# Performance work log

Hardware: AMD Instinct MI355X
Metric: run time of the kernel (lower is better)

## Reference

```python
import jax, jax.numpy as jnp
import numpy as np

N, D, H, O, P = 50000, 256, 512, 64, 1024


def setup_inputs() -> dict:
    key = jax.random.key(0)
    ks = jax.random.split(key, 9)
    x = jax.random.normal(ks[0], (N, D), dtype=jnp.float32)
    W1 = jax.random.normal(ks[1], (H, D), dtype=jnp.float32) / np.sqrt(D)
    b1 = jax.random.normal(ks[2], (H,), dtype=jnp.float32) * 0.01
    W2 = jax.random.normal(ks[3], (O, H), dtype=jnp.float32) / np.sqrt(H)
    b2 = jax.random.normal(ks[4], (O,), dtype=jnp.float32) * 0.01
    ap = jax.random.randint(ks[5], (P,), 0, N, dtype=jnp.int32)
    p = jax.random.randint(ks[6], (P,), 0, N, dtype=jnp.int32)
    an = jax.random.randint(ks[7], (P,), 0, N, dtype=jnp.int32)
    n = jax.random.randint(ks[8], (P,), 0, N, dtype=jnp.int32)
    return {"x": x, "W1": W1, "b1": b1, "W2": W2, "b2": b2,
            "ap": ap, "p": p, "an": an, "n": n}


def reference(x, W1, b1, W2, b2, ap, p, an, n):
    """ContrastiveHessianCalculator.compute_hessian, loss_func='contrastive_full',
    wrt='weight', shape='diagonal', speed='half' (exact GGN diag), for the nnj net
    Linear(D,H) -> Tanh -> Linear(H,O).

    For a pair (x1,x2) the combined diag m0 - 2*m1 + m2 equals
    diag((J1-J2)^T (J1-J2)) where Ji = d f(xi)/d params. Closed form per layer:
      W1[i,j]: S11_i*x1_j^2 - 2*S12_i*x1_j*x2_j + S22_i*x2_j^2,
               Sab_i = tanh'(z1a)_i * tanh'(z1b)_i * sum_o W2[o,i]^2
      b1[i]:   S11_i - 2*S12_i + S22_i
      W2[i,j]: (h1_j - h2_j)^2  (independent of output row i)
      b2[i]:   0  (bias Jacobians of the two branches cancel)
    Per-layer diags are flattened [weight, bias] and concatenated (torch.cat(.., dim=1)),
    then summed over the pair batch; return sum(pos) - sum(neg).
    """
    c = jnp.sum(W2 * W2, axis=0)  # [H]

    def pair_hess_diag(ia, ib):
        xa = x[ia]            # [P, D]
        xb = x[ib]            # [P, D]
        ha = jnp.tanh(xa @ W1.T + b1)   # [P, H]
        hb = jnp.tanh(xb @ W1.T + b1)
        da = 1.0 - ha * ha              # tanh' at x_a, [P, H]
        db = 1.0 - hb * hb
        S11 = da * da * c               # [P, H]
        S12 = da * db * c
        S22 = db * db * c
        # W1 diag: [P, H, D]
        W1d = (S11[:, :, None] * (xa * xa)[:, None, :]
               - 2.0 * S12[:, :, None] * (xa * xb)[:, None, :]
               + S22[:, :, None] * (xb * xb)[:, None, :])
        b1d = S11 - 2.0 * S12 + S22      # [P, H]
        hd = (ha - hb) ** 2              # [P, H]
        W2d = jnp.broadcast_to(hd[:, None, :], (hd.shape[0], O, H))  # [P, O, H]
        b2d = jnp.zeros((hd.shape[0], O), dtype=hd.dtype)
        flat = jnp.concatenate([W1d.reshape(hd.shape[0], -1), b1d,
                                W2d.reshape(hd.shape[0], -1), b2d], axis=1)
        return jnp.sum(flat, axis=0)     # sum over pair batch -> [n_params]

    pos = pair_hess_diag(ap, p)
    neg = pair_hess_diag(an, n)
    return pos - neg
```

## Files before the change

kernel.cpp:

```cpp
#include <hip/hip_runtime.h>
#include <math.h>

#define DD_ 256
#define HH_ 512
#define OO_ 64

typedef __attribute__((ext_vector_type(8))) short bf16x8s;
typedef __attribute__((ext_vector_type(4))) float f32x4;

__device__ __forceinline__ unsigned short f2bf(float f) {
    unsigned u = __float_as_uint(f);
    u += 0x7FFF + ((u >> 16) & 1);
    return (unsigned short)(u >> 16);
}
__device__ __forceinline__ float bf2f(unsigned short h) {
    return __uint_as_float(((unsigned)h) << 16);
}
__device__ __forceinline__ int swz4(int r, int g) {
    return g ^ (r & 3) ^ ((r >> 2) & 3);
}
__device__ __forceinline__ float fast_tanh(float z) {
    float e = __expf(2.f * z);
    return 1.f - __fdividef(2.f, e + 1.f);
}

__global__ __launch_bounds__(256) void k_mega(
    const float* __restrict__ x, const float* __restrict__ W1,
    const float* __restrict__ b1, const float* __restrict__ W2,
    const int* __restrict__ ap, const int* __restrict__ pI,
    const int* __restrict__ an, const int* __restrict__ nI,
    short* __restrict__ Mt, short* __restrict__ Xt,
    float* __restrict__ pb1, float* __restrict__ phd) {
    const int t = threadIdx.x;
    const int bb = blockIdx.x;
    if (bb < 512) {
        __shared__ short Ah[64 * 32], Al[64 * 32], Bh[64 * 32], Bl[64 * 32];
        __shared__ float ht[64][67];
        __shared__ int sidx[64];
        const int n0 = (bb & 7) * 64;
        const int ry = bb >> 3;
        const int s = ry >> 5;
        const int p0 = (ry & 31) * 32;
        const int* IA = s ? an : ap;
        const int* IB = s ? nI : pI;
        if (t < 32) sidx[t] = IA[p0 + t];
        else if (t < 64) sidx[t] = IB[p0 + t - 32];
        __syncthreads();
        const int row = t >> 2, q = t & 3;
        const int l = t & 63, w = t >> 6;
        const int wm = w >> 1, wn = w & 1;
        const int lm = l & 15, g = l >> 4;
        const int sw = swz4(row, q);
        const float* srcA = x + (size_t)sidx[row] * DD_ + q * 8;
        const float* srcB = W1 + (size_t)(n0 + row) * DD_ + q * 8;
        float4 pa0 = *(const float4*)srcA;
        float4 pa1 = *(const float4*)(srcA + 4);
        float4 pb0 = *(const float4*)srcB;
        float4 pb1v = *(const float4*)(srcB + 4);
        f32x4 acc[2][2] = {};
        for (int k0 = 0; k0 < DD_; k0 += 32) {
            {
                float f[8] = {pa0.x, pa0.y, pa0.z, pa0.w, pa1.x, pa1.y, pa1.z, pa1.w};
                bf16x8s hi, lo;
                #pragma unroll
                for (int e = 0; e < 8; ++e) {
                    unsigned short hh = f2bf(f[e]);
                    hi[e] = (short)hh;
                    lo[e] = (short)f2bf(f[e] - bf2f(hh));
                }
                *(bf16x8s*)(&Ah[(row * 4 + sw) * 8]) = hi;
                *(bf16x8s*)(&Al[(row * 4 + sw) * 8]) = lo;
            }
            {
                float f[8] = {pb0.x, pb0.y, pb0.z, pb0.w, pb1v.x, pb1v.y, pb1v.z, pb1v.w};
                bf16x8s hi, lo;
                #pragma unroll
                for (int e = 0; e < 8; ++e) {
                    unsigned short hh = f2bf(f[e]);
                    hi[e] = (short)hh;
                    lo[e] = (short)f2bf(f[e] - bf2f(hh));
                }
                *(bf16x8s*)(&Bh[(row * 4 + sw) * 8]) = hi;
                *(bf16x8s*)(&Bl[(row * 4 + sw) * 8]) = lo;
            }
            __syncthreads();
            if (k0 + 32 < DD_) {
                pa0 = *(const float4*)(srcA + k0 + 32);
                pa1 = *(const float4*)(srcA + k0 + 36);
                pb0 = *(const float4*)(srcB + k0 + 32);
                pb1v = *(const float4*)(srcB + k0 + 36);
            }
            bf16x8s ah[2], al[2], bh[2], bl[2];
            #pragma unroll
            for (int mi = 0; mi < 2; ++mi) {
                int r = wm * 32 + mi * 16 + lm;
                ah[mi] = *(const bf16x8s*)(&Ah[(r * 4 + swz4(r, g)) * 8]);
                al[mi] = *(const bf16x8s*)(&Al[(r * 4 + swz4(r, g)) * 8]);
            }
            #pragma unroll
            for (int nj = 0; nj < 2; ++nj) {
                int r = wn * 32 + nj * 16 + lm;
                bh[nj] = *(const bf16x8s*)(&Bh[(r * 4 + swz4(r, g)) * 8]);
                bl[nj] = *(const bf16x8s*)(&Bl[(r * 4 + swz4(r, g)) * 8]);
            }
            #pragma unroll
            for (int mi = 0; mi < 2; ++mi)
                #pragma unroll
                for (int nj = 0; nj < 2; ++nj) {
                    acc[mi][nj] = __builtin_amdgcn_mfma_f32_16x16x32_bf16(ah[mi], bh[nj], acc[mi][nj], 0, 0, 0);
                    acc[mi][nj] = __builtin_amdgcn_mfma_f32_16x16x32_bf16(ah[mi], bl[nj], acc[mi][nj], 0, 0, 0);
                    acc[mi][nj] = __builtin_amdgcn_mfma_f32_16x16x32_bf16(al[mi], bh[nj], acc[mi][nj], 0, 0, 0);
                }
            __syncthreads();
        }
        #pragma unroll
        for (int mi = 0; mi < 2; ++mi)
            #pragma unroll
            for (int nj = 0; nj < 2; ++nj) {
                int jl = wn * 32 + nj * 16 + lm;
                float bv = b1[n0 + jl];
                #pragma unroll
                for (int qq = 0; qq < 4; ++qq) {
                    int r = wm * 32 + mi * 16 + g * 4 + qq;
                    ht[r][jl] = fast_tanh(acc[mi][nj][qq] + bv);
                }
            }
        __syncthreads();
        const int il = t >> 2, pq = t & 3;
        float ci = 0.f;
        #pragma unroll 8
        for (int o = 0; o < OO_; ++o) { float wv = W2[o * HH_ + n0 + il]; ci += wv * wv; }
        const float sgn = s ? -1.f : 1.f;
        float b1p = 0.f, hdp = 0.f;
        bf16x8s v0, v1, v2;
        #pragma unroll
        for (int pp = 0; pp < 8; ++pp) {
            int pl = pq * 8 + pp;
            float ha = ht[pl][il];
            float hb = ht[pl + 32][il];
            float da = 1.f - ha * ha, db = 1.f - hb * hb;
            float s11 = sgn * (da * da * ci);
            float s12 = sgn * (-2.f * da * db * ci);
            float s22 = sgn * (db * db * ci);
            v0[pp] = (short)f2bf(s11);
            v1[pp] = (short)f2bf(s12);
            v2[pp] = (short)f2bf(s22);
            b1p += s11 + s12 + s22;
            float d = ha - hb;
            hdp += sgn * d * d;
        }
        size_t base = (size_t)(n0 + il) * 6144 + s * 1024 + p0 + pq * 8;
        *(bf16x8s*)(&Mt[base]) = v0;
        *(bf16x8s*)(&Mt[base + 2048]) = v1;
        *(bf16x8s*)(&Mt[base + 4096]) = v2;
        b1p += __shfl_xor(b1p, 1); b1p += __shfl_xor(b1p, 2);
        hdp += __shfl_xor(hdp, 1); hdp += __shfl_xor(hdp, 2);
        if (pq == 0) { pb1[ry * HH_ + n0 + il] = b1p; phd[ry * HH_ + n0 + il] = hdp; }
    } else {
        __shared__ int sia[64], sib[64];
        const int b2 = bb - 512;
        const int jblk = b2 >> 5, pblk = b2 & 31;
        const int j = jblk * 64 + (t >> 2), pq = t & 3;
        const int p0 = pblk * 64;
        const int s = p0 >> 10;
        const int* IA = s ? an : ap;
        const int* IB = s ? nI : pI;
        if (t < 64) sia[t] = IA[(p0 & 1023) + t];
        else if (t < 128) sib[t - 64] = IB[(p0 & 1023) + (t - 64)];
        __syncthreads();
        short xv[3][16];
        #pragma unroll
        for (int pp = 0; pp < 16; ++pp) {
            int pl = pq * 16 + pp;
            float xa = x[(size_t)sia[pl] * DD_ + j];
            float xb = x[(size_t)sib[pl] * DD_ + j];
            xv[0][pp] = (short)f2bf(xa * xa);
            xv[1][pp] = (short)f2bf(xa * xb);
            xv[2][pp] = (short)f2bf(xb * xb);
        }
        size_t base = (size_t)j * 6144 + p0 + pq * 16;
        #pragma unroll
        for (int term = 0; term < 3; ++term) {
            bf16x8s v0, v1;
            #pragma unroll
            for (int e = 0; e < 8; ++e) { v0[e] = xv[term][e]; v1[e] = xv[term][e + 8]; }
            *(bf16x8s*)(&Xt[base + (size_t)term * 2048]) = v0;
            *(bf16x8s*)(&Xt[base + (size_t)term * 2048 + 8]) = v1;
        }
    }
}

__global__ __launch_bounds__(256) void k_gemm2(
    const short* __restrict__ Mt, const short* __restrict__ Xt,
    float* __restrict__ part) {
    __shared__ short As[64 * 32], Bs[64 * 32];
    const int t = threadIdx.x;
    const int j0 = blockIdx.x * 64;
    const int i0 = blockIdx.y * 64;
    const int kb = blockIdx.z;
    const int row = t >> 2, q = t & 3;
    const int l = t & 63, w = t >> 6;
    const int wm = w >> 1, wn = w & 1;
    const int lm = l & 15, g = l >> 4;
    const int sw = swz4(row, q);
    const short* srcA = &Mt[(size_t)(i0 + row) * 6144 + kb * 384 + q * 8];
    const short* srcB = &Xt[(size_t)(j0 + row) * 6144 + kb * 384 + q * 8];
    bf16x8s ra = *(const bf16x8s*)srcA;
    bf16x8s rb = *(const bf16x8s*)srcB;
    f32x4 acc[2][2] = {};
    for (int ks = 0; ks < 12; ++ks) {
        *(bf16x8s*)(&As[(row * 4 + sw) * 8]) = ra;
        *(bf16x8s*)(&Bs[(row * 4 + sw) * 8]) = rb;
        __syncthreads();
        if (ks < 11) {
            ra = *(const bf16x8s*)(srcA + (ks + 1) * 32);
            rb = *(const bf16x8s*)(srcB + (ks + 1) * 32);
        }
        bf16x8s a[2], b[2];
        #pragma unroll
        for (int mi = 0; mi < 2; ++mi) {
            int r = wm * 32 + mi * 16 + lm;
            a[mi] = *(const bf16x8s*)(&As[(r * 4 + swz4(r, g)) * 8]);
        }
        #pragma unroll
        for (int nj = 0; nj < 2; ++nj) {
            int r = wn * 32 + nj * 16 + lm;
            b[nj] = *(const bf16x8s*)(&Bs[(r * 4 + swz4(r, g)) * 8]);
        }
        #pragma unroll
        for (int mi = 0; mi < 2; ++mi)
            #pragma unroll
            for (int nj = 0; nj < 2; ++nj)
                acc[mi][nj] = __builtin_amdgcn_mfma_f32_16x16x32_bf16(a[mi], b[nj], acc[mi][nj], 0, 0, 0);
        __syncthreads();
    }
    #pragma unroll
    for (int mi = 0; mi < 2; ++mi)
        #pragma unroll
        for (int nj = 0; nj < 2; ++nj) {
            int j = j0 + wn * 32 + nj * 16 + lm;
            #pragma unroll
            for (int qq = 0; qq < 4; ++qq) {
                int i = i0 + wm * 32 + mi * 16 + g * 4 + qq;
                part[((size_t)kb * HH_ + i) * DD_ + j] = acc[mi][nj][qq];
            }
        }
}

__global__ void k_tail(const float* __restrict__ part, const float* __restrict__ pb1,
                       const float* __restrict__ phd, float* __restrict__ out) {
    const int gid = blockIdx.x * 256 + threadIdx.x;
    const int HD4 = 32768;
    f32x4* out4 = (f32x4*)out;
    if (gid < HD4) {
        f32x4 sv = {};
        #pragma unroll
        for (int kb = 0; kb < 16; ++kb)
            sv += *(const f32x4*)(&part[(size_t)kb * 131072 + gid * 4]);
        out4[gid] = sv;
    } else if (gid < HD4 + 128) {
        const int i4 = gid - HD4;
        f32x4 sv = {};
        for (int k2 = 0; k2 < 64; ++k2)
            sv += *(const f32x4*)(&pb1[k2 * HH_ + i4 * 4]);
        out4[HD4 + i4] = sv;
    } else if (gid < HD4 + 256) {
        const int i4 = gid - HD4 - 128;
        f32x4 sv = {};
        for (int k2 = 0; k2 < 64; ++k2)
            sv += *(const f32x4*)(&phd[k2 * HH_ + i4 * 4]);
        #pragma unroll 8
        for (int o = 0; o < OO_; ++o)
            out4[HD4 + 128 + o * 128 + i4] = sv;
    } else if (gid < HD4 + 272) {
        f32x4 z = {};
        out4[41088 + gid - HD4 - 256] = z;
    }
}

extern "C" void kernel_launch(void* const* d_in, const int* in_sizes, int n_in,
                              void* d_out, int out_size, void* d_ws, size_t ws_size,
                              hipStream_t stream) {
    const float* x  = (const float*)d_in[0];
    const float* W1 = (const float*)d_in[1];
    const float* b1 = (const float*)d_in[2];
    const float* W2 = (const float*)d_in[3];
    const int* ap = (const int*)d_in[5];
    const int* pI = (const int*)d_in[6];
    const int* an = (const int*)d_in[7];
    const int* nI = (const int*)d_in[8];
    float* out = (float*)d_out;
    float* ws = (float*)d_ws;

    float* part = ws;
    short* Mt   = (short*)(ws + 2097152);
    short* Xt   = (short*)(ws + 3670016);
    float* pb1  = ws + 4456448;
    float* phd  = ws + 4489216;

    k_mega<<<dim3(640), dim3(256), 0, stream>>>(x, W1, b1, W2, ap, pI, an, nI,
                                                Mt, Xt, pb1, phd);
    k_gemm2<<<dim3(4, 8, 16), dim3(256), 0, stream>>>(Mt, Xt, part);
    k_tail<<<dim3(130), dim3(256), 0, stream>>>(part, pb1, phd, out);
}
```

Before: 33.81 us.

## Double-buffer LDS tiles, pack bf16 conversions, fold Xt production into GEMM1 blocks

Both GEMM loops now use double-buffered shared memory, so each iteration needs one barrier instead of two and the next tile's conversion and store overlap the current MFMAs. The fp32-to-bf16 hi/lo split uses packed two-element conversion intrinsics. The separate 128 blocks that built the Xt squared-input matrix are removed, and every one of the 512 GEMM1 blocks now also writes a quarter of an Xt tile, which balances work across blocks. The cost is twice the shared memory per block and smaller 8-byte Xt stores with indices read straight from global memory.

```diff
diff --git a/kernel.cpp b/kernel.cpp
--- a/kernel.cpp
+++ b/kernel.cpp
@@ -1,4 +1,5 @@
 #include <hip/hip_runtime.h>
+#include <hip/hip_bf16.h>
 #include <math.h>
 
 #define DD_ 256
@@ -6,15 +7,31 @@
 #define OO_ 64
 
 typedef __attribute__((ext_vector_type(8))) short bf16x8s;
+typedef __attribute__((ext_vector_type(4))) short bf16x4s;
 typedef __attribute__((ext_vector_type(4))) float f32x4;
+typedef __attribute__((ext_vector_type(4))) unsigned int u32x4;
 
 __device__ __forceinline__ unsigned short f2bf(float f) {
     unsigned u = __float_as_uint(f);
     u += 0x7FFF + ((u >> 16) & 1);
     return (unsigned short)(u >> 16);
 }
-__device__ __forceinline__ float bf2f(unsigned short h) {
-    return __uint_as_float(((unsigned)h) << 16);
+__device__ __forceinline__ unsigned pk2(float a, float b) {
+    __hip_bfloat162 h = __float22bfloat162_rn(make_float2(a, b));
+    return *reinterpret_cast<unsigned*>(&h);
+}
+__device__ __forceinline__ void cvt8hl(const float4& v0, const float4& v1,
+                                       u32x4& hi, u32x4& lo) {
+    float f[8] = {v0.x, v0.y, v0.z, v0.w, v1.x, v1.y, v1.z, v1.w};
+    #pragma unroll
+    for (int e = 0; e < 4; ++e) {
+        float a = f[2 * e], b = f[2 * e + 1];
+        unsigned h = pk2(a, b);
+        float ra = a - __uint_as_float(h << 16);
+        float rb = b - __uint_as_float(h & 0xFFFF0000u);
+        hi[e] = h;
+        lo[e] = pk2(ra, rb);
+    }
 }
 __device__ __forceinline__ int swz4(int r, int g) {
     return g ^ (r & 3) ^ ((r >> 2) & 3);
@@ -31,101 +48,95 @@
     const int* __restrict__ an, const int* __restrict__ nI,
     short* __restrict__ Mt, short* __restrict__ Xt,
     float* __restrict__ pb1, float* __restrict__ phd) {
+    __shared__ short Ah[2][64 * 32], Al[2][64 * 32];
+    __shared__ short Bh[2][64 * 32], Bl[2][64 * 32];
+    __shared__ float ht[64][67];
+    __shared__ int sidx[64];
     const int t = threadIdx.x;
     const int bb = blockIdx.x;
-    if (bb < 512) {
-        __shared__ short Ah[64 * 32], Al[64 * 32], Bh[64 * 32], Bl[64 * 32];
-        __shared__ float ht[64][67];
-        __shared__ int sidx[64];
-        const int n0 = (bb & 7) * 64;
-        const int ry = bb >> 3;
-        const int s = ry >> 5;
-        const int p0 = (ry & 31) * 32;
-        const int* IA = s ? an : ap;
-        const int* IB = s ? nI : pI;
-        if (t < 32) sidx[t] = IA[p0 + t];
-        else if (t < 64) sidx[t] = IB[p0 + t - 32];
+    const int n0 = (bb & 7) * 64;
+    const int ry = bb >> 3;
+    const int s = ry >> 5;
+    const int p0 = (ry & 31) * 32;
+    const int* IA = s ? an : ap;
+    const int* IB = s ? nI : pI;
+    if (t < 32) sidx[t] = IA[p0 + t];
+    else if (t < 64) sidx[t] = IB[p0 + t - 32];
+    __syncthreads();
+    const int row = t >> 2, q = t & 3;
+    const int l = t & 63, w = t >> 6;
+    const int wm = w >> 1, wn = w & 1;
+    const int lm = l & 15, g = l >> 4;
+    const int sw = swz4(row, q);
+    const int stIdx = (row * 4 + sw) * 8;
+    const float* srcA = x + (size_t)sidx[row] * DD_ + q * 8;
+    const float* srcB = W1 + (size_t)(n0 + row) * DD_ + q * 8;
+    {
+        float4 a0 = *(const float4*)srcA;
+        float4 a1 = *(const float4*)(srcA + 4);
+        float4 b0 = *(const float4*)srcB;
+        float4 b1q = *(const float4*)(srcB + 4);
+        u32x4 hi, lo;
+        cvt8hl(a0, a1, hi, lo);
+        *(u32x4*)(&Ah[0][stIdx]) = hi; *(u32x4*)(&Al[0][stIdx]) = lo;
+        cvt8hl(b0, b1q, hi, lo);
+        *(u32x4*)(&Bh[0][stIdx]) = hi; *(u32x4*)(&Bl[0][stIdx]) = lo;
+    }
+    f32x4 acc[2][2] = {};
+    #pragma unroll 2
+    for (int ks = 0; ks < 8; ++ks) {
+        const int cur = ks & 1;
         __syncthreads();
-        const int row = t >> 2, q = t & 3;
-        const int l = t & 63, w = t >> 6;
-        const int wm = w >> 1, wn = w & 1;
-        const int lm = l & 15, g = l >> 4;
-        const int sw = swz4(row, q);
-        const float* srcA = x + (size_t)sidx[row] * DD_ + q * 8;
-        const float* srcB = W1 + (size_t)(n0 + row) * DD_ + q * 8;
-        float4 pa0 = *(const float4*)srcA;
-        float4 pa1 = *(const float4*)(srcA + 4);
-        float4 pb0 = *(const float4*)srcB;
-        float4 pb1v = *(const float4*)(srcB + 4);
-        f32x4 acc[2][2] = {};
-        for (int k0 = 0; k0 < DD_; k0 += 32) {
-            {
-                float f[8] = {pa0.x, pa0.y, pa0.z, pa0.w, pa1.x, pa1.y, pa1.z, pa1.w};
-                bf16x8s hi, lo;
-                #pragma unroll
-                for (int e = 0; e < 8; ++e) {
-                    unsigned short hh = f2bf(f[e]);
-                    hi[e] = (short)hh;
-                    lo[e] = (short)f2bf(f[e] - bf2f(hh));
-                }
-                *(bf16x8s*)(&Ah[(row * 4 + sw) * 8]) = hi;
-                *(bf16x8s*)(&Al[(row * 4 + sw) * 8]) = lo;
+        float4 na0, na1, nb0, nb1q;
+        if (ks < 7) {
+            na0 = *(const float4*)(srcA + (ks + 1) * 32);
+            na1 = *(const float4*)(srcA + (ks + 1) * 32 + 4);
+            nb0 = *(const float4*)(srcB + (ks + 1) * 32);
+            nb1q = *(const float4*)(srcB + (ks + 1) * 32 + 4);
+        }
+        bf16x8s ah[2], al[2], bh[2], bl[2];
+        #pragma unroll
+        for (int mi = 0; mi < 2; ++mi) {
+            int r = wm * 32 + mi * 16 + lm;
+            ah[mi] = *(const bf16x8s*)(&Ah[cur][(r * 4 + swz4(r, g)) * 8]);
+            al[mi] = *(const bf16x8s*)(&Al[cur][(r * 4 + swz4(r, g)) * 8]);
+        }
+        #pragma unroll
+        for (int nj = 0; nj < 2; ++nj) {
+            int r = wn * 32 + nj * 16 + lm;
+            bh[nj] = *(const bf16x8s*)(&Bh[cur][(r * 4 + swz4(r, g)) * 8]);
+            bl[nj] = *(const bf16x8s*)(&Bl[cur][(r * 4 + swz4(r, g)) * 8]);
+        }
+        #pragma unroll
+        for (int mi = 0; mi < 2; ++mi)
+            #pragma unroll
+            for (int nj = 0; nj < 2; ++nj) {
+                acc[mi][nj] = __builtin_amdgcn_mfma_f32_16x16x32_bf16(ah[mi], bh[nj], acc[mi][nj], 0, 0, 0);
+                acc[mi][nj] = __builtin_amdgcn_mfma_f32_16x16x32_bf16(ah[mi], bl[nj], acc[mi][nj], 0, 0, 0);
+                acc[mi][nj] = __builtin_amdgcn_mfma_f32_16x16x32_bf16(al[mi], bh[nj], acc[mi][nj], 0, 0, 0);
             }
-            {
-                float f[8] = {pb0.x, pb0.y, pb0.z, pb0.w, pb1v.x, pb1v.y, pb1v.z, pb1v.w};
-                bf16x8s hi, lo;
-                #pragma unroll
-                for (int e = 0; e < 8; ++e) {
-                    unsigned short hh = f2bf(f[e]);
-                    hi[e] = (short)hh;
-                    lo[e] = (short)f2bf(f[e] - bf2f(hh));
-                }
-                *(bf16x8s*)(&Bh[(row * 4 + sw) * 8]) = hi;
-                *(bf16x8s*)(&Bl[(row * 4 + sw) * 8]) = lo;
+        if (ks < 7) {
+            u32x4 hi, lo;
+            cvt8hl(na0, na1, hi, lo);
+            *(u32x4*)(&Ah[cur ^ 1][stIdx]) = hi; *(u32x4*)(&Al[cur ^ 1][stIdx]) = lo;
+            cvt8hl(nb0, nb1q, hi, lo);
+            *(u32x4*)(&Bh[cur ^ 1][stIdx]) = hi; *(u32x4*)(&Bl[cur ^ 1][stIdx]) = lo;
+        }
+    }
+    #pragma unroll
+    for (int mi = 0; mi < 2; ++mi)
+        #pragma unroll
+        for (int nj = 0; nj < 2; ++nj) {
+            int jl = wn * 32 + nj * 16 + lm;
+            float bv = b1[n0 + jl];
+            #pragma unroll
+            for (int qq = 0; qq < 4; ++qq) {
+                int r = wm * 32 + mi * 16 + g * 4 + qq;
+                ht[r][jl] = fast_tanh(acc[mi][nj][qq] + bv);
             }
-            __syncthreads();
-            if (k0 + 32 < DD_) {
-                pa0 = *(const float4*)(srcA + k0 + 32);
-                pa1 = *(const float4*)(srcA + k0 + 36);
-                pb0 = *(const float4*)(srcB + k0 + 32);
-                pb1v = *(const float4*)(srcB + k0 + 36);
-            }
-            bf16x8s ah[2], al[2], bh[2], bl[2];
-            #pragma unroll
-            for (int mi = 0; mi < 2; ++mi) {
-                int r = wm * 32 + mi * 16 + lm;
-                ah[mi] = *(const bf16x8s*)(&Ah[(r * 4 + swz4(r, g)) * 8]);
-                al[mi] = *(const bf16x8s*)(&Al[(r * 4 + swz4(r, g)) * 8]);
-            }
-            #pragma unroll
-            for (int nj = 0; nj < 2; ++nj) {
-                int r = wn * 32 + nj * 16 + lm;
-                bh[nj] = *(const bf16x8s*)(&Bh[(r * 4 + swz4(r, g)) * 8]);
-                bl[nj] = *(const bf16x8s*)(&Bl[(r * 4 + swz4(r, g)) * 8]);
-            }
-            #pragma unroll
-            for (int mi = 0; mi < 2; ++mi)
-                #pragma unroll
-                for (int nj = 0; nj < 2; ++nj) {
-                    acc[mi][nj] = __builtin_amdgcn_mfma_f32_16x16x32_bf16(ah[mi], bh[nj], acc[mi][nj], 0, 0, 0);
-                    acc[mi][nj] = __builtin_amdgcn_mfma_f32_16x16x32_bf16(ah[mi], bl[nj], acc[mi][nj], 0, 0, 0);
-                    acc[mi][nj] = __builtin_amdgcn_mfma_f32_16x16x32_bf16(al[mi], bh[nj], acc[mi][nj], 0, 0, 0);
-                }
-            __syncthreads();
-        }
-        #pragma unroll
-        for (int mi = 0; mi < 2; ++mi)
-            #pragma unroll
-            for (int nj = 0; nj < 2; ++nj) {
-                int jl = wn * 32 + nj * 16 + lm;
-                float bv = b1[n0 + jl];
-                #pragma unroll
-                for (int qq = 0; qq < 4; ++qq) {
-                    int r = wm * 32 + mi * 16 + g * 4 + qq;
-                    ht[r][jl] = fast_tanh(acc[mi][nj][qq] + bv);
-                }
-            }
-        __syncthreads();
+        }
+    __syncthreads();
+    {
         const int il = t >> 2, pq = t & 3;
         float ci = 0.f;
         #pragma unroll 8
@@ -156,36 +167,36 @@
         b1p += __shfl_xor(b1p, 1); b1p += __shfl_xor(b1p, 2);
         hdp += __shfl_xor(hdp, 1); hdp += __shfl_xor(hdp, 2);
         if (pq == 0) { pb1[ry * HH_ + n0 + il] = b1p; phd[ry * HH_ + n0 + il] = hdp; }
-    } else {
-        __shared__ int sia[64], sib[64];
-        const int b2 = bb - 512;
-        const int jblk = b2 >> 5, pblk = b2 & 31;
-        const int j = jblk * 64 + (t >> 2), pq = t & 3;
-        const int p0 = pblk * 64;
-        const int s = p0 >> 10;
-        const int* IA = s ? an : ap;
-        const int* IB = s ? nI : pI;
-        if (t < 64) sia[t] = IA[(p0 & 1023) + t];
-        else if (t < 128) sib[t - 64] = IB[(p0 & 1023) + (t - 64)];
-        __syncthreads();
-        short xv[3][16];
-        #pragma unroll
-        for (int pp = 0; pp < 16; ++pp) {
-            int pl = pq * 16 + pp;
-            float xa = x[(size_t)sia[pl] * DD_ + j];
-            float xb = x[(size_t)sib[pl] * DD_ + j];
+    }
+    {
+        const int xb = bb >> 2;
+        const int quarter = bb & 3;
+        const int jblk = xb >> 5, pblk = xb & 31;
+        const int j = jblk * 64 + (t >> 2);
+        const int pq = t & 3;
+        const int p0x = pblk * 64;
+        const int sX = p0x >> 10;
+        const int* IA2 = sX ? an : ap;
+        const int* IB2 = sX ? nI : pI;
+        const int pbase = (p0x & 1023) + quarter * 16 + pq * 4;
+        short xv[3][4];
+        #pragma unroll
+        for (int pp = 0; pp < 4; ++pp) {
+            int ia = IA2[pbase + pp];
+            int ib = IB2[pbase + pp];
+            float xa = x[(size_t)ia * DD_ + j];
+            float xbv = x[(size_t)ib * DD_ + j];
             xv[0][pp] = (short)f2bf(xa * xa);
-            xv[1][pp] = (short)f2bf(xa * xb);
-            xv[2][pp] = (short)f2bf(xb * xb);
-        }
-        size_t base = (size_t)j * 6144 + p0 + pq * 16;
+            xv[1][pp] = (short)f2bf(xa * xbv);
+            xv[2][pp] = (short)f2bf(xbv * xbv);
+        }
+        size_t base = (size_t)j * 6144 + p0x + quarter * 16 + pq * 4;
         #pragma unroll
         for (int term = 0; term < 3; ++term) {
-            bf16x8s v0, v1;
-            #pragma unroll
-            for (int e = 0; e < 8; ++e) { v0[e] = xv[term][e]; v1[e] = xv[term][e + 8]; }
-            *(bf16x8s*)(&Xt[base + (size_t)term * 2048]) = v0;
-            *(bf16x8s*)(&Xt[base + (size_t)term * 2048 + 8]) = v1;
+            bf16x4s v;
+            #pragma unroll
+            for (int e = 0; e < 4; ++e) v[e] = xv[term][e];
+            *(bf16x4s*)(&Xt[base + (size_t)term * 2048]) = v;
         }
     }
 }
@@ -193,7 +204,7 @@
 __global__ __launch_bounds__(256) void k_gemm2(
     const short* __restrict__ Mt, const short* __restrict__ Xt,
     float* __restrict__ part) {
-    __shared__ short As[64 * 32], Bs[64 * 32];
+    __shared__ short As[2][64 * 32], Bs[2][64 * 32];
     const int t = threadIdx.x;
     const int j0 = blockIdx.x * 64;
     const int i0 = blockIdx.y * 64;
@@ -203,36 +214,43 @@
     const int wm = w >> 1, wn = w & 1;
     const int lm = l & 15, g = l >> 4;
     const int sw = swz4(row, q);
+    const int stIdx = (row * 4 + sw) * 8;
     const short* srcA = &Mt[(size_t)(i0 + row) * 6144 + kb * 384 + q * 8];
     const short* srcB = &Xt[(size_t)(j0 + row) * 6144 + kb * 384 + q * 8];
-    bf16x8s ra = *(const bf16x8s*)srcA;
-    bf16x8s rb = *(const bf16x8s*)srcB;
+    {
+        *(bf16x8s*)(&As[0][stIdx]) = *(const bf16x8s*)srcA;
+        *(bf16x8s*)(&Bs[0][stIdx]) = *(const bf16x8s*)srcB;
+    }
     f32x4 acc[2][2] = {};
+    #pragma unroll 2
     for (int ks = 0; ks < 12; ++ks) {
-        *(bf16x8s*)(&As[(row * 4 + sw) * 8]) = ra;
-        *(bf16x8s*)(&Bs[(row * 4 + sw) * 8]) = rb;
+        const int cur = ks & 1;
         __syncthreads();
+        bf16x8s na, nb;
         if (ks < 11) {
-            ra = *(const bf16x8s*)(srcA + (ks + 1) * 32);
-            rb = *(const bf16x8s*)(srcB + (ks + 1) * 32);
+            na = *(const bf16x8s*)(srcA + (ks + 1) * 32);
+            nb = *(const bf16x8s*)(srcB + (ks + 1) * 32);
         }
         bf16x8s a[2], b[2];
         #pragma unroll
         for (int mi = 0; mi < 2; ++mi) {
             int r = wm * 32 + mi * 16 + lm;
-            a[mi] = *(const bf16x8s*)(&As[(r * 4 + swz4(r, g)) * 8]);
+            a[mi] = *(const bf16x8s*)(&As[cur][(r * 4 + swz4(r, g)) * 8]);
         }
         #pragma unroll
         for (int nj = 0; nj < 2; ++nj) {
             int r = wn * 32 + nj * 16 + lm;
-            b[nj] = *(const bf16x8s*)(&Bs[(r * 4 + swz4(r, g)) * 8]);
+            b[nj] = *(const bf16x8s*)(&Bs[cur][(r * 4 + swz4(r, g)) * 8]);
         }
         #pragma unroll
         for (int mi = 0; mi < 2; ++mi)
             #pragma unroll
             for (int nj = 0; nj < 2; ++nj)
                 acc[mi][nj] = __builtin_amdgcn_mfma_f32_16x16x32_bf16(a[mi], b[nj], acc[mi][nj], 0, 0, 0);
-        __syncthreads();
+        if (ks < 11) {
+            *(bf16x8s*)(&As[cur ^ 1][stIdx]) = na;
+            *(bf16x8s*)(&Bs[cur ^ 1][stIdx]) = nb;
+        }
     }
     #pragma unroll
     for (int mi = 0; mi < 2; ++mi)
@@ -298,7 +316,7 @@
     float* pb1  = ws + 4456448;
     float* phd  = ws + 4489216;
 
-    k_mega<<<dim3(640), dim3(256), 0, stream>>>(x, W1, b1, W2, ap, pI, an, nI,
+    k_mega<<<dim3(512), dim3(256), 0, stream>>>(x, W1, b1, W2, ap, pI, an, nI,
                                                 Mt, Xt, pb1, phd);
     k_gemm2<<<dim3(4, 8, 16), dim3(256), 0, stream>>>(Mt, Xt, part);
     k_tail<<<dim3(130), dim3(256), 0, stream>>>(part, pb1, phd, out);
```

New measurement: 36.46 us. 1.08x slower.
